# Kernel tuning notes

Measured on AMD Instinct MI355X. Metric: run time of the kernel, lower is better.

## Reference

```python
import jax, jax.numpy as jnp
import numpy as np

N_NODES = 50000
N_EDGES = 800000


def setup_inputs() -> dict:
    key = jax.random.key(0)
    ks = jax.random.split(key, 16)
    def W(k, shape, fan_in):
        return jax.random.normal(k, shape, dtype=jnp.float32) / np.sqrt(fan_in)
    return {
        "x": jax.random.normal(ks[0], (N_NODES, 64), dtype=jnp.float32),
        "edge_attr": jax.random.uniform(ks[1], (N_EDGES, 1), dtype=jnp.float32),
        "edge_index": jax.random.randint(ks[2], (2, N_EDGES), 0, N_NODES, dtype=jnp.int64),
        "W_pre1": W(ks[3], (65, 16), 65), "b_pre1": jnp.zeros((16,), jnp.float32),
        "W_net1": W(ks[4], (16, 16), 16), "b_net1": jnp.zeros((16,), jnp.float32),
        "W_out1": W(ks[5], (16, 16), 16), "b_out1": jnp.zeros((16,), jnp.float32),
        "W_pre2": W(ks[6], (17, 16), 17), "b_pre2": jnp.zeros((16,), jnp.float32),
        "W_net2": W(ks[7], (16, 16), 16), "b_net2": jnp.zeros((16,), jnp.float32),
        "W_out2": W(ks[8], (16, 16), 16), "b_out2": jnp.zeros((16,), jnp.float32),
    }


def _mpnn_conv(x, edge_index, edge_attr, Wp, bp, Wn, bn, Wo, bo, activation):
    """Edge-gather MLP + scatter-max aggregation (MpnnConv)."""
    src, dst = edge_index[0], edge_index[1]
    # per-edge message: Linear(concat(x_src, edge_attr)) -> relu -> net (Linear)
    m = jnp.concatenate([x[src], edge_attr], axis=1) @ Wp + bp      # [E, mid]
    m = jax.nn.relu(m)
    m = m @ Wn + bn                                                  # [E, mid]
    # scatter-max to destination nodes; empty segments -> 0
    agg = jax.ops.segment_max(m, dst, num_segments=x.shape[0])      # [N, mid]
    agg = jnp.where(jnp.isfinite(agg), agg, 0.0)
    out = agg @ Wo + bo                                              # [N, out]
    return activation(out) if activation is not None else out


def reference(x, edge_attr, edge_index,
              W_pre1, b_pre1, W_net1, b_net1, W_out1, b_out1,
              W_pre2, b_pre2, W_net2, b_net2, W_out2, b_out2):
    # eval mode: dropout is identity
    h = _mpnn_conv(x, edge_index, edge_attr, W_pre1, b_pre1, W_net1, b_net1,
                   W_out1, b_out1, jax.nn.elu)
    h = jax.nn.elu(h)  # outer F.elu in Net.forward
    h = _mpnn_conv(h, edge_index, edge_attr, W_pre2, b_pre2, W_net2, b_net2,
                   W_out2, b_out2, None)
    return jax.nn.log_softmax(h, axis=1)
```

## Files before the change

kernel.cpp:

```cpp
#include <hip/hip_runtime.h>
#include <math.h>

#define NN 50000
#define NE 800000
#define BSHIFT 7
#define BNODES 128
#define NB 391
#define NBB 200
#define EPB 4000
#define PRE_BLOCKS 196

__device__ __forceinline__ float elu1(float v) {
    return v > 0.0f ? v : expm1f(v);
}

__global__ void setup_kernel(const int* __restrict__ ei, int* __restrict__ HM,
                             const float* __restrict__ x,
                             const float* __restrict__ Wp,
                             const float* __restrict__ bp,
                             float* __restrict__ P1) {
    __shared__ unsigned hist[NB];
    __shared__ float sW[64 * 16];
    __shared__ float sb[16];
    if (blockIdx.x < NBB) {
        for (int i = threadIdx.x; i < NB; i += 256) hist[i] = 0;
        __syncthreads();
        int base = blockIdx.x * EPB;
        for (int i = threadIdx.x; i < EPB; i += 256) {
            int d = ei[NE + base + i];
            atomicAdd(&hist[d >> BSHIFT], 1u);
        }
        __syncthreads();
        for (int b = threadIdx.x; b < NB; b += 256)
            HM[b * NBB + blockIdx.x] = (int)hist[b];
    } else {
        for (int i = threadIdx.x; i < 64 * 16; i += 256) sW[i] = Wp[i];
        if (threadIdx.x < 16) sb[threadIdx.x] = bp[threadIdx.x];
        __syncthreads();
        int n = (blockIdx.x - NBB) * 256 + threadIdx.x;
        if (n >= NN) return;
        float acc[16];
#pragma unroll
        for (int k = 0; k < 16; ++k) acc[k] = sb[k];
        const float4* xr = (const float4*)(x + (size_t)n * 64);
#pragma unroll
        for (int j4 = 0; j4 < 16; ++j4) {
            float4 xv = xr[j4];
            const float* w = &sW[j4 * 4 * 16];
#pragma unroll
            for (int k = 0; k < 16; ++k) acc[k] += xv.x * w[k];
#pragma unroll
            for (int k = 0; k < 16; ++k) acc[k] += xv.y * w[16 + k];
#pragma unroll
            for (int k = 0; k < 16; ++k) acc[k] += xv.z * w[32 + k];
#pragma unroll
            for (int k = 0; k < 16; ++k) acc[k] += xv.w * w[48 + k];
        }
        float4* o = (float4*)(P1 + (size_t)n * 16);
        o[0] = make_float4(acc[0], acc[1], acc[2], acc[3]);
        o[1] = make_float4(acc[4], acc[5], acc[6], acc[7]);
        o[2] = make_float4(acc[8], acc[9], acc[10], acc[11]);
        o[3] = make_float4(acc[12], acc[13], acc[14], acc[15]);
    }
}

__global__ void row_scan_kernel(int* __restrict__ HM, int* __restrict__ rowsum) {
    __shared__ int s[256];
    int t = threadIdx.x, b = blockIdx.x;
    int v = (t < NBB) ? HM[b * NBB + t] : 0;
    s[t] = v;
    __syncthreads();
#pragma unroll
    for (int off = 1; off < 256; off <<= 1) {
        int tmp = (t >= off) ? s[t - off] : 0;
        __syncthreads();
        s[t] += tmp;
        __syncthreads();
    }
    if (t < NBB) HM[b * NBB + t] = s[t] - v;
    if (t == 255) rowsum[b] = s[255];
}

__global__ void scan_rows_kernel(const int* __restrict__ rowsum, int* __restrict__ bstart) {
    __shared__ int s[512];
    int t = threadIdx.x;
    int v = (t < NB) ? rowsum[t] : 0;
    s[t] = v;
    __syncthreads();
#pragma unroll
    for (int off = 1; off < 512; off <<= 1) {
        int tmp = (t >= off) ? s[t - off] : 0;
        __syncthreads();
        s[t] += tmp;
        __syncthreads();
    }
    if (t < NB) bstart[t] = s[t] - v;
    if (t == 511) bstart[NB] = s[511];
}

__global__ void bin2_kernel(const int* __restrict__ ei, const float* __restrict__ ea,
                            const int* __restrict__ HM, const int* __restrict__ bstart,
                            int2* __restrict__ sp1) {
    __shared__ unsigned cur[NB];
    for (int b = threadIdx.x; b < NB; b += 256)
        cur[b] = (unsigned)(bstart[b] + HM[b * NBB + blockIdx.x]);
    __syncthreads();
    int base = blockIdx.x * EPB;
    for (int i = threadIdx.x; i < EPB; i += 256) {
        int e = base + i;
        int d = ei[NE + e];
        int srcv = ei[e];
        int b = d >> BSHIFT;
        int dl = d & (BNODES - 1);
        unsigned pos = atomicAdd(&cur[b], 1u);
        sp1[pos] = make_int2(srcv | (dl << 16), __float_as_int(ea[e]));
    }
}

__global__ void sort_kernel(const int2* __restrict__ sp1,
                            const int* __restrict__ bstart,
                            int2* __restrict__ sp2,
                            int* __restrict__ start,
                            int* __restrict__ perm) {
    __shared__ unsigned hist[BNODES];
    __shared__ int s[256];
    __shared__ unsigned dcnt[64];
    __shared__ unsigned dcur[64];
    __shared__ int dlof[BNODES];
    __shared__ int soff[BNODES];
    __shared__ unsigned cur[BNODES];
    __shared__ int sdeg[BNODES];
    int tid = threadIdx.x;
    int b = blockIdx.x;
    int e0 = bstart[b], e1 = bstart[b + 1];
    if (tid < BNODES) hist[tid] = 0;
    if (tid < 64) dcnt[tid] = 0;
    __syncthreads();
    for (int i = e0 + tid; i < e1; i += 256) {
        int dl = (sp1[i].x >> 16) & (BNODES - 1);
        atomicAdd(&hist[dl], 1u);
    }
    __syncthreads();
    if (tid < BNODES) {
        int key = min((int)hist[tid], 63);
        atomicAdd(&dcnt[key], 1u);
    }
    __syncthreads();
    int v = (tid < 64) ? (int)dcnt[tid] : 0;
    s[tid] = v;
    __syncthreads();
#pragma unroll
    for (int off = 1; off < 64; off <<= 1) {
        int tmp = (tid >= off) ? s[tid - off] : 0;
        __syncthreads();
        s[tid] += tmp;
        __syncthreads();
    }
    if (tid < 64) dcur[tid] = (unsigned)(s[tid] - v);
    __syncthreads();
    if (tid < BNODES) {
        int key = min((int)hist[tid], 63);
        int rank = (int)atomicAdd(&dcur[key], 1u);
        dlof[rank] = tid;
    }
    __syncthreads();
    if (tid < BNODES) sdeg[tid] = (int)hist[dlof[tid]];
    __syncthreads();
    int v2 = (tid < BNODES) ? sdeg[tid] : 0;
    s[tid] = v2;
    __syncthreads();
#pragma unroll
    for (int off = 1; off < 128; off <<= 1) {
        int tmp = (tid >= off) ? s[tid - off] : 0;
        __syncthreads();
        s[tid] += tmp;
        __syncthreads();
    }
    if (tid < BNODES) {
        int off = s[tid] - v2;
        soff[tid] = off;
        start[b * BNODES + tid] = e0 + off;
        perm[b * BNODES + tid] = b * BNODES + dlof[tid];
    }
    __syncthreads();
    if (tid < BNODES) cur[dlof[tid]] = (unsigned)(e0 + soff[tid]);
    if (b == NB - 1 && tid == 0) start[NB * BNODES] = e1;
    __syncthreads();
    for (int i = e0 + tid; i < e1; i += 256) {
        int2 rec = sp1[i];
        int dl = (rec.x >> 16) & (BNODES - 1);
        int pos = (int)atomicAdd(&cur[dl], 1u);
        sp2[pos] = make_int2(rec.x & 0xFFFF, rec.y);
    }
}

template <int MODE>
__global__ void __launch_bounds__(256, 4)
gather_kernel(const long long* __restrict__ sp,
              const int* __restrict__ start,
              const int* __restrict__ perm,
              const float* __restrict__ Pin,
              const float* __restrict__ wl,
              const float* __restrict__ Wn,
              const float* __restrict__ bn,
              const float* __restrict__ Wo,
              const float* __restrict__ bo,
              const float* __restrict__ Wpn,
              const float* __restrict__ bpn,
              float* __restrict__ out) {
    __shared__ float swl[16], sbn[16], sbo[16], sbpn[16];
    __shared__ float sWnT[16][17];
    __shared__ float sWo[256], sWpn[256];
    __shared__ float sAgg[32][17];
    int tid = threadIdx.x;
    if (tid < 256) {
        sWnT[tid & 15][tid >> 4] = Wn[tid];
        sWo[tid] = Wo[tid];
        if (MODE == 0) sWpn[tid] = Wpn[tid];
    }
    if (tid < 16) {
        swl[tid] = wl[tid]; sbn[tid] = bn[tid]; sbo[tid] = bo[tid];
        if (MODE == 0) sbpn[tid] = bpn[tid];
    }
    __syncthreads();

    int l  = tid >> 3;
    int g  = tid & 3;
    int hi = (tid >> 2) & 1;
    int r = blockIdx.x * 32 + l;
    int n = perm[r];
    bool valid = (n < NN);

    float acc[4] = {-INFINITY, -INFINITY, -INFINITY, -INFINITY};
    int s0 = start[r], s1 = start[r + 1];

    float wl0 = swl[g * 4 + 0], wl1 = swl[g * 4 + 1],
          wl2 = swl[g * 4 + 2], wl3 = swl[g * 4 + 3];
    float bn0 = sbn[g * 4 + 0], bn1 = sbn[g * 4 + 1],
          bn2 = sbn[g * 4 + 2], bn3 = sbn[g * 4 + 3];
    bool g1 = (g & 1) != 0, g2 = (g & 2) != 0;

    float wreg[64];
#pragma unroll
    for (int c = 0; c < 16; ++c) {
#pragma unroll
        for (int j = 0; j < 4; ++j) wreg[c * 4 + j] = sWnT[c][g * 4 + j];
    }

    int s = s0 + hi;
    while (s < s1) {
        int sB = (s + 2 < s1) ? (s + 2) : s;
        long long rA = sp[s];
        long long rB = sp[sB];
        int srcA = (int)(rA & 0xFFFFFFFFll);
        int srcB = (int)(rB & 0xFFFFFFFFll);
        float4 qA = ((const float4*)(Pin + (size_t)srcA * 16))[g];
        float4 qB = ((const float4*)(Pin + (size_t)srcB * 16))[g];
        float aA = __int_as_float((int)(rA >> 32));
        float aB = __int_as_float((int)(rB >> 32));
        s += 4;

#pragma unroll
        for (int e = 0; e < 2; ++e) {
            float4 cv = e ? qB : qA;
            float a = e ? aB : aA;
            float t0 = fmaxf(fmaf(a, wl0, cv.x), 0.0f);
            float t1 = fmaxf(fmaf(a, wl1, cv.y), 0.0f);
            float t2 = fmaxf(fmaf(a, wl2, cv.z), 0.0f);
            float t3 = fmaxf(fmaf(a, wl3, cv.w), 0.0f);
            float m[16];
#pragma unroll
            for (int c = 0; c < 16; ++c) {
                float o = t0 * wreg[c * 4 + 0];
                o = fmaf(t1, wreg[c * 4 + 1], o);
                o = fmaf(t2, wreg[c * 4 + 2], o);
                o = fmaf(t3, wreg[c * 4 + 3], o);
                m[c] = o;
            }
            float h[8];
#pragma unroll
            for (int c = 0; c < 8; ++c) {
                float send = g2 ? m[c] : m[c + 8];
                float recv = __shfl_xor(send, 2, 64);
                h[c] = (g2 ? m[c + 8] : m[c]) + recv;
            }
            float send, recv, r0, r1, r2, r3;
            send = g1 ? h[0] : h[4]; recv = __shfl_xor(send, 1, 64); r0 = (g1 ? h[4] : h[0]) + recv;
            send = g1 ? h[1] : h[5]; recv = __shfl_xor(send, 1, 64); r1 = (g1 ? h[5] : h[1]) + recv;
            send = g1 ? h[2] : h[6]; recv = __shfl_xor(send, 1, 64); r2 = (g1 ? h[6] : h[2]) + recv;
            send = g1 ? h[3] : h[7]; recv = __shfl_xor(send, 1, 64); r3 = (g1 ? h[7] : h[3]) + recv;
            acc[0] = fmaxf(acc[0], r0 + bn0);
            acc[1] = fmaxf(acc[1], r1 + bn1);
            acc[2] = fmaxf(acc[2], r2 + bn2);
            acc[3] = fmaxf(acc[3], r3 + bn3);
        }
    }
#pragma unroll
    for (int q = 0; q < 4; ++q) acc[q] = fmaxf(acc[q], __shfl_xor(acc[q], 4, 64));

    bool empty = (s1 == s0);
#pragma unroll
    for (int q = 0; q < 4; ++q) sAgg[l][g * 4 + q] = empty ? 0.0f : acc[q];
    __syncthreads();

    if (MODE == 0) {
        float h[4];
#pragma unroll
        for (int q = 0; q < 4; ++q) {
            int c = g * 4 + q;
            float o = sbo[c];
#pragma unroll
            for (int j = 0; j < 16; ++j) o = fmaf(sAgg[l][j], sWo[j * 16 + c], o);
            h[q] = elu1(elu1(o));
        }
        __syncthreads();
        if (hi == 0) {
#pragma unroll
            for (int q = 0; q < 4; ++q) sAgg[l][g * 4 + q] = h[q];
        }
        __syncthreads();
        float p[4];
#pragma unroll
        for (int q = 0; q < 4; ++q) {
            int c = g * 4 + q;
            float o = sbpn[c];
#pragma unroll
            for (int k = 0; k < 16; ++k) o = fmaf(sAgg[l][k], sWpn[k * 16 + c], o);
            p[q] = o;
        }
        if (valid && hi == 0) {
            float4* op = (float4*)(out + (size_t)n * 16 + g * 4);
            *op = make_float4(p[0], p[1], p[2], p[3]);
        }
    } else {
        float oo[4];
#pragma unroll
        for (int q = 0; q < 4; ++q) {
            int c = g * 4 + q;
            float o = sbo[c];
#pragma unroll
            for (int j = 0; j < 16; ++j) o = fmaf(sAgg[l][j], sWo[j * 16 + c], o);
            oo[q] = o;
        }
        __syncthreads();
        if (hi == 0) {
#pragma unroll
            for (int q = 0; q < 4; ++q) sAgg[l][g * 4 + q] = oo[q];
        }
        __syncthreads();
        float mx = -INFINITY;
#pragma unroll
        for (int j = 0; j < 16; ++j) mx = fmaxf(mx, sAgg[l][j]);
        float sum = 0.0f;
#pragma unroll
        for (int j = 0; j < 16; ++j) sum += expf(sAgg[l][j] - mx);
        float ls = logf(sum) + mx;
        if (valid && hi == 0) {
            float4* op = (float4*)(out + (size_t)n * 16 + g * 4);
            *op = make_float4(oo[0] - ls, oo[1] - ls, oo[2] - ls, oo[3] - ls);
        }
    }
}

extern "C" void kernel_launch(void* const* d_in, const int* in_sizes, int n_in,
                              void* d_out, int out_size, void* d_ws, size_t ws_size,
                              hipStream_t stream) {
    const float* x         = (const float*)d_in[0];
    const float* edge_attr = (const float*)d_in[1];
    const int*   edge_index= (const int*)  d_in[2];
    const float* W_pre1 = (const float*)d_in[3];
    const float* b_pre1 = (const float*)d_in[4];
    const float* W_net1 = (const float*)d_in[5];
    const float* b_net1 = (const float*)d_in[6];
    const float* W_out1 = (const float*)d_in[7];
    const float* b_out1 = (const float*)d_in[8];
    const float* W_pre2 = (const float*)d_in[9];
    const float* b_pre2 = (const float*)d_in[10];
    const float* W_net2 = (const float*)d_in[11];
    const float* b_net2 = (const float*)d_in[12];
    const float* W_out2 = (const float*)d_in[13];
    const float* b_out2 = (const float*)d_in[14];

    char* ws = (char*)d_ws;
    int2*  sp1    = (int2*) (ws);
    int2*  sp2    = (int2*) (ws + 6400000);
    float* P1     = (float*)(ws + 12800000);
    float* P2     = (float*)(ws + 16000000);
    int*   HM     = (int*)  (ws + 19200000);
    int*   bstart = (int*)  (ws + 19520000);
    int*   rowsum = (int*)  (ws + 19524000);
    int*   start  = (int*)  (ws + 19528000);
    int*   perm   = (int*)  (ws + 19728256);

    const int GATH_BLOCKS = (NB * BNODES) / 32;

    setup_kernel<<<NBB + PRE_BLOCKS, 256, 0, stream>>>(edge_index, HM, x, W_pre1, b_pre1, P1);
    row_scan_kernel<<<NB, 256, 0, stream>>>(HM, rowsum);
    scan_rows_kernel<<<1, 512, 0, stream>>>(rowsum, bstart);
    bin2_kernel<<<NBB, 256, 0, stream>>>(edge_index, edge_attr, HM, bstart, sp1);
    sort_kernel<<<NB, 256, 0, stream>>>(sp1, bstart, sp2, start, perm);

    gather_kernel<0><<<GATH_BLOCKS, 256, 0, stream>>>((const long long*)sp2, start, perm, P1,
        W_pre1 + 64 * 16, W_net1, b_net1, W_out1, b_out1, W_pre2, b_pre2, P2);

    gather_kernel<1><<<GATH_BLOCKS, 256, 0, stream>>>((const long long*)sp2, start, perm, P2,
        W_pre2 + 16 * 16, W_net2, b_net2, W_out2, b_out2, nullptr, nullptr,
        (float*)d_out);
}
```

Baseline: 95.50 us.

## Fuse histogram scans into bin kernel, removing two scan launches

Removes the separate row-scan and row-sum scan kernels and has each bin2 block recompute the per-bucket totals and its own prefix from the histogram matrix, followed by a block-wide scan over the buckets. This cuts two kernel launches and their serialization points. In exchange, every one of the 200 blocks redundantly reads the whole 391x200 histogram with a serial loop per thread, and the block size doubles to 512.

```diff
diff --git a/kernel.cpp b/kernel.cpp
--- a/kernel.cpp
+++ b/kernel.cpp
@@ -64,49 +64,42 @@
     }
 }
 
-__global__ void row_scan_kernel(int* __restrict__ HM, int* __restrict__ rowsum) {
-    __shared__ int s[256];
-    int t = threadIdx.x, b = blockIdx.x;
-    int v = (t < NBB) ? HM[b * NBB + t] : 0;
-    s[t] = v;
-    __syncthreads();
-#pragma unroll
-    for (int off = 1; off < 256; off <<= 1) {
-        int tmp = (t >= off) ? s[t - off] : 0;
-        __syncthreads();
-        s[t] += tmp;
-        __syncthreads();
-    }
-    if (t < NBB) HM[b * NBB + t] = s[t] - v;
-    if (t == 255) rowsum[b] = s[255];
-}
-
-__global__ void scan_rows_kernel(const int* __restrict__ rowsum, int* __restrict__ bstart) {
+__global__ void bin2_kernel(const int* __restrict__ ei, const float* __restrict__ ea,
+                            const int* __restrict__ HM,
+                            int* __restrict__ bstart,
+                            int2* __restrict__ sp1) {
     __shared__ int s[512];
-    int t = threadIdx.x;
-    int v = (t < NB) ? rowsum[t] : 0;
-    s[t] = v;
+    __shared__ unsigned cur[NB];
+    __shared__ int sbs[NB];
+    int tid = threadIdx.x;
+    int blk = blockIdx.x;
+    int total = 0, pre = 0;
+    if (tid < NB) {
+        const int* row = HM + tid * NBB;
+        for (int k = 0; k < NBB; ++k) {
+            if (k == blk) pre = total;
+            total += row[k];
+        }
+    }
+    s[tid] = total;
     __syncthreads();
 #pragma unroll
     for (int off = 1; off < 512; off <<= 1) {
-        int tmp = (t >= off) ? s[t - off] : 0;
-        __syncthreads();
-        s[t] += tmp;
-        __syncthreads();
-    }
-    if (t < NB) bstart[t] = s[t] - v;
-    if (t == 511) bstart[NB] = s[511];
-}
-
-__global__ void bin2_kernel(const int* __restrict__ ei, const float* __restrict__ ea,
-                            const int* __restrict__ HM, const int* __restrict__ bstart,
-                            int2* __restrict__ sp1) {
-    __shared__ unsigned cur[NB];
-    for (int b = threadIdx.x; b < NB; b += 256)
-        cur[b] = (unsigned)(bstart[b] + HM[b * NBB + blockIdx.x]);
-    __syncthreads();
-    int base = blockIdx.x * EPB;
-    for (int i = threadIdx.x; i < EPB; i += 256) {
+        int tmp = (tid >= off) ? s[tid - off] : 0;
+        __syncthreads();
+        s[tid] += tmp;
+        __syncthreads();
+    }
+    if (tid < NB) {
+        int base = s[tid] - total;
+        sbs[tid] = base;
+        cur[tid] = (unsigned)(base + pre);
+        if (blk == 0) bstart[tid] = base;
+    }
+    if (blk == 0 && tid == 0) bstart[NB] = s[511];
+    __syncthreads();
+    int base = blk * EPB;
+    for (int i = tid; i < EPB; i += 512) {
         int e = base + i;
         int d = ei[NE + e];
         int srcv = ei[e];
@@ -388,16 +381,13 @@
     float* P2     = (float*)(ws + 16000000);
     int*   HM     = (int*)  (ws + 19200000);
     int*   bstart = (int*)  (ws + 19520000);
-    int*   rowsum = (int*)  (ws + 19524000);
     int*   start  = (int*)  (ws + 19528000);
     int*   perm   = (int*)  (ws + 19728256);
 
     const int GATH_BLOCKS = (NB * BNODES) / 32;
 
     setup_kernel<<<NBB + PRE_BLOCKS, 256, 0, stream>>>(edge_index, HM, x, W_pre1, b_pre1, P1);
-    row_scan_kernel<<<NB, 256, 0, stream>>>(HM, rowsum);
-    scan_rows_kernel<<<1, 512, 0, stream>>>(rowsum, bstart);
-    bin2_kernel<<<NBB, 256, 0, stream>>>(edge_index, edge_attr, HM, bstart, sp1);
+    bin2_kernel<<<NBB, 512, 0, stream>>>(edge_index, edge_attr, HM, bstart, sp1);
     sort_kernel<<<NB, 256, 0, stream>>>(sp1, bstart, sp2, start, perm);
 
     gather_kernel<0><<<GATH_BLOCKS, 256, 0, stream>>>((const long long*)sp2, start, perm, P1,
```

Result: faster. 93.57 us (-2.0%).
